# Performance work log

Hardware: AMD Instinct MI355X
Metric: run time of the kernel (lower is better)

## Reference

```python
import jax, jax.numpy as jnp
import numpy as np

B = 1024

def _back_mask(mask_out, selh, selw, s, k, hin, win):
    # Mark which input positions (of this conv) are touched by sampled k x k patches.
    hc, wc = hin - k + 1, win - k + 1
    m = np.zeros((hin, win), np.float32)
    ho, wo = mask_out.shape
    for i in range(ho):
        for j in range(wo):
            if mask_out[i, j] > 0:
                ph = min(i * s + int(selh[i, j]), hc - 1)
                pw = min(j * s + int(selw[i, j]), wc - 1)
                m[ph:ph + k, pw:pw + k] = 1.0
    return m


def setup_inputs() -> dict:
    key = jax.random.key(0)
    ks = jax.random.split(key, 10)
    rng = np.random.default_rng(1)
    # stochastic pooling offsets, top-down as in the torch forward
    selh3 = rng.integers(0, 4, (1, 1)).astype(np.int32)
    selw3 = rng.integers(0, 4, (1, 1)).astype(np.int32)
    mask3 = np.ones((1, 1), np.float32)
    mask2 = _back_mask(mask3, selh3, selw3, s=4, k=3, hin=6, win=6)
    selh2 = rng.integers(0, 2, (6, 6)).astype(np.int32)
    selw2 = rng.integers(0, 2, (6, 6)).astype(np.int32)
    mask1 = _back_mask(mask2, selh2, selw2, s=2, k=3, hin=14, win=14)
    selh1 = rng.integers(0, 2, (14, 14)).astype(np.int32)
    selw1 = rng.integers(0, 2, (14, 14)).astype(np.int32)
    sc = 0.05
    return {
        "x": jax.random.normal(ks[0], (B, 3, 32, 32), jnp.float32),
        "W1": jax.random.normal(ks[1], (200, 3, 5, 5), jnp.float32) * sc,
        "b1": jax.random.normal(ks[2], (200,), jnp.float32) * sc,
        "W2": jax.random.normal(ks[3], (400, 200, 3, 3), jnp.float32) * sc,
        "b2": jax.random.normal(ks[4], (400,), jnp.float32) * sc,
        "W3": jax.random.normal(ks[5], (800, 400, 3, 3), jnp.float32) * sc,
        "b3": jax.random.normal(ks[6], (800,), jnp.float32) * sc,
        "fc_w": jax.random.normal(ks[7], (10, 800), jnp.float32) * sc,
        "fc_b": jax.random.normal(ks[8], (10,), jnp.float32) * sc,
        "selh1": jnp.asarray(selh1), "selw1": jnp.asarray(selw1),
        "selh2": jnp.asarray(selh2), "selw2": jnp.asarray(selw2),
        "selh3": jnp.asarray(selh3), "selw3": jnp.asarray(selw3),
        "mask1": jnp.asarray(mask1), "mask2": jnp.asarray(mask2),
        "mask3": jnp.asarray(mask3),
    }


def _sconv_avg(x, W, b, selh, selw, mask, k, s):
    # Stochastic conv+avgpool: compute stride-1 conv only at one sampled location
    # per pooling window, zero at masked-out output positions.
    Bq, C, H, Wd = x.shape
    hc, wc = H - k + 1, Wd - k + 1
    ho, wo = selh.shape
    ph = jnp.minimum(jnp.arange(ho)[:, None] * s + selh, hc - 1)  # (ho,wo)
    pw = jnp.minimum(jnp.arange(wo)[None, :] * s + selw, wc - 1)
    rows = ph[:, :, :, None] if False else (ph[..., None] + jnp.arange(k))  # (ho,wo,k)
    cols = pw[..., None] + jnp.arange(k)                                    # (ho,wo,k)
    # gather sampled k x k patches -> (B,C,ho,wo,k,k)
    patch = x[:, :, rows[:, :, :, None], cols[:, :, None, :]]
    out = jnp.einsum('bcxyij,ocij->boxy', patch, W) + b[None, :, None, None]
    return out * mask[None, None, :, :]


def reference(x, W1, b1, W2, b2, W3, b3, fc_w, fc_b,
              selh1, selw1, selh2, selw2, selh3, selw3,
              mask1, mask2, mask3):
    h = jax.nn.relu(_sconv_avg(x, W1, b1, selh1, selw1, mask1, k=5, s=2))   # (B,200,14,14)
    h = jax.nn.relu(_sconv_avg(h, W2, b2, selh2, selw2, mask2, k=3, s=2))   # (B,400,6,6)
    h = jax.nn.relu(_sconv_avg(h, W3, b3, selh3, selw3, mask3, k=3, s=4))   # (B,800,1,1)
    h = h.reshape(h.shape[0], -1)                                           # (B,800)
    return h @ fc_w.T + fc_b
```

## Files before the change

kernel.cpp:

```cpp
#include <hip/hip_runtime.h>


#define H1B_OFF 0ULL
#define W2B_OFF 80281600ULL
#define P3_OFF  81944576ULL
#define W3B_OFF 89415680ULL
#define H3_OFF  95485952ULL
#define W1T_OFF 98762752ULL

typedef unsigned short u16;
typedef short bf16x8 __attribute__((ext_vector_type(8)));
typedef float f32x4 __attribute__((ext_vector_type(4)));

__device__ __forceinline__ u16 f2bf(float f) {
    union { float f; unsigned int u; } v; v.f = f;
    unsigned int u = v.u + 0x7FFFu + ((v.u >> 16) & 1u);
    return (u16)(u >> 16);
}

__global__ __launch_bounds__(256) void wprep(
    const float* __restrict__ W1, const float* __restrict__ W2, const float* __restrict__ W3,
    float* __restrict__ W1t, u16* __restrict__ W2b, u16* __restrict__ W3b)
{
    int idx = blockIdx.x * 256 + threadIdx.x;
    if (idx < 20480) {
        int kk = idx / 256, oc = idx % 256;
        float v = 0.0f;
        if (oc < 200 && kk < 75) v = W1[oc * 75 + kk];
        W1t[idx] = v;
    } else if (idx < 20480 + 831488) {
        int j = idx - 20480;
        int oc = j / 1856, kk = j % 1856;
        float v = 0.0f;
        if (oc < 400 && kk < 1800) {
            int k3 = kk / 200, c = kk % 200;
            v = W2[oc * 1800 + c * 9 + k3];
        }
        W2b[j] = f2bf(v);
    } else if (idx < 20480 + 831488 + 3035136) {
        int j = idx - 20480 - 831488;
        int oc = j / 3648, kk = j % 3648;
        float v = 0.0f;
        if (oc < 800 && kk < 3600) {
            int k3 = kk / 400, c = kk % 400;
            v = W3[oc * 3600 + c * 9 + k3];
        }
        W3b[j] = f2bf(v);
    }
}

__global__ __launch_bounds__(256) void l1_kernel(
    const float* __restrict__ x, const float* __restrict__ W1t, const float* __restrict__ b1,
    const int* __restrict__ selh, const int* __restrict__ selw, const float* __restrict__ mask,
    u16* __restrict__ h1b)
{
    const int pos = blockIdx.x;
    const float m = mask[pos];
    if (m == 0.0f) return;
    const int i = pos / 14, j = pos % 14;
    const int b0 = blockIdx.y * 16;
    const int tid = threadIdx.x;
    const int ph = min(i * 2 + selh[pos], 27);
    const int pw = min(j * 2 + selw[pos], 27);

    __shared__ __align__(16) float patch[16 * 80];
    for (int e = tid; e < 1280; e += 256) {
        int u = e / 80, kk = e % 80;
        float v = 0.0f;
        if (kk < 75) {
            int c = kk / 25, d = kk % 25;
            v = x[((size_t)(b0 + u) * 3 + c) * 1024 + (ph + d / 5) * 32 + (pw + d % 5)];
        }
        patch[e] = v;
    }
    __syncthreads();

    const int g = tid & 63;
    const int us = tid >> 6;
    const float4* w4 = reinterpret_cast<const float4*>(W1t);
    const float4* p4 = reinterpret_cast<const float4*>(patch);

    float4 acc[4];
#pragma unroll
    for (int uu = 0; uu < 4; ++uu) acc[uu] = make_float4(0.f, 0.f, 0.f, 0.f);

#pragma unroll 2
    for (int q = 0; q < 20; ++q) {
        float4 w0 = w4[(q * 4 + 0) * 64 + g];
        float4 w1 = w4[(q * 4 + 1) * 64 + g];
        float4 w2 = w4[(q * 4 + 2) * 64 + g];
        float4 w3 = w4[(q * 4 + 3) * 64 + g];
#pragma unroll
        for (int uu = 0; uu < 4; ++uu) {
            float4 p = p4[(us * 4 + uu) * 20 + q];
            acc[uu].x = fmaf(w0.x, p.x, acc[uu].x);
            acc[uu].y = fmaf(w0.y, p.x, acc[uu].y);
            acc[uu].z = fmaf(w0.z, p.x, acc[uu].z);
            acc[uu].w = fmaf(w0.w, p.x, acc[uu].w);
            acc[uu].x = fmaf(w1.x, p.y, acc[uu].x);
            acc[uu].y = fmaf(w1.y, p.y, acc[uu].y);
            acc[uu].z = fmaf(w1.z, p.y, acc[uu].z);
            acc[uu].w = fmaf(w1.w, p.y, acc[uu].w);
            acc[uu].x = fmaf(w2.x, p.z, acc[uu].x);
            acc[uu].y = fmaf(w2.y, p.z, acc[uu].y);
            acc[uu].z = fmaf(w2.z, p.z, acc[uu].z);
            acc[uu].w = fmaf(w2.w, p.z, acc[uu].w);
            acc[uu].x = fmaf(w3.x, p.w, acc[uu].x);
            acc[uu].y = fmaf(w3.y, p.w, acc[uu].y);
            acc[uu].z = fmaf(w3.z, p.w, acc[uu].z);
            acc[uu].w = fmaf(w3.w, p.w, acc[uu].w);
        }
    }

    if (g < 50) {
        float4 bv = reinterpret_cast<const float4*>(b1)[g];
#pragma unroll
        for (int uu = 0; uu < 4; ++uu) {
            int b = b0 + us * 4 + uu;
            ushort4 o;
            o.x = f2bf(fmaxf((acc[uu].x + bv.x) * m, 0.0f));
            o.y = f2bf(fmaxf((acc[uu].y + bv.y) * m, 0.0f));
            o.z = f2bf(fmaxf((acc[uu].z + bv.z) * m, 0.0f));
            o.w = f2bf(fmaxf((acc[uu].w + bv.w) * m, 0.0f));
            *reinterpret_cast<ushort4*>(&h1b[((size_t)b * 196 + pos) * 200 + g * 4]) = o;
        }
    }
}

__global__ __launch_bounds__(256) void gemm_l2(
    const u16* __restrict__ h1b, const u16* __restrict__ B, const float* __restrict__ bias,
    const int* __restrict__ selh2, const int* __restrict__ selw2,
    const int* __restrict__ selh3, const int* __restrict__ selw3,
    u16* __restrict__ P3)
{
    const int KP = 1856, NKT = 29;
    const int m0 = blockIdx.x * 64, n0 = blockIdx.y * 64;
    const int tid = threadIdx.x;
    const int lane = tid & 63, wid = tid >> 6;
    const int wm = wid >> 1, wn = wid & 1;

    __shared__ u16 Asm[64][72];
    __shared__ u16 Bsm[64][72];

    f32x4 zero = {0.f, 0.f, 0.f, 0.f};
    f32x4 acc00 = zero, acc01 = zero, acc10 = zero, acc11 = zero;

    const int ar = tid >> 3, ac = tid & 7;
    const int ph2 = min(selh3[0], 3), pw2 = min(selw3[0], 3);
    int mr0 = m0 + ar, mr1 = mr0 + 32;
    int bq0 = mr0 / 9, p0 = mr0 - bq0 * 9;
    int bq1 = mr1 / 9, p1 = mr1 - bq1 * 9;
    int pos0 = (ph2 + p0 / 3) * 6 + (pw2 + p0 % 3);
    int pos1 = (ph2 + p1 / 3) * 6 + (pw2 + p1 % 3);
    int base0 = bq0 * 196 + min(2 * (pos0 / 6) + selh2[pos0], 11) * 14
                          + min(2 * (pos0 % 6) + selw2[pos0], 11);
    int base1 = bq1 * 196 + min(2 * (pos1 / 6) + selh2[pos1], 11) * 14
                          + min(2 * (pos1 % 6) + selw2[pos1], 11);
    auto gatherA = [&](int kt, int base) -> uint4 {
        int chunk = kt * 8 + ac;
        if (chunk >= 225) return make_uint4(0u, 0u, 0u, 0u);
        int k3 = chunk / 25, c8 = chunk - k3 * 25;
        int srow = base + (k3 / 3) * 14 + (k3 - (k3 / 3) * 3);
        return *reinterpret_cast<const uint4*>(h1b + (size_t)srow * 200 + c8 * 8);
    };
    const uint4* Bg0 = reinterpret_cast<const uint4*>(B + (size_t)(n0 + ar) * KP + ac * 8);
    const uint4* Bg1 = reinterpret_cast<const uint4*>(B + (size_t)(n0 + ar + 32) * KP + ac * 8);
    uint4* As0 = reinterpret_cast<uint4*>(&Asm[ar][ac * 8]);
    uint4* As1 = reinterpret_cast<uint4*>(&Asm[ar + 32][ac * 8]);
    uint4* Bs0 = reinterpret_cast<uint4*>(&Bsm[ar][ac * 8]);
    uint4* Bs1 = reinterpret_cast<uint4*>(&Bsm[ar + 32][ac * 8]);

    uint4 ra0 = gatherA(0, base0), ra1 = gatherA(0, base1);
    uint4 rb0 = Bg0[0], rb1 = Bg1[0];
    const int r = lane & 15, ks = lane >> 4;
    for (int kt = 0; kt < NKT; ++kt) {
        __syncthreads();
        *As0 = ra0; *As1 = ra1; *Bs0 = rb0; *Bs1 = rb1;
        __syncthreads();
        if (kt + 1 < NKT) {
            ra0 = gatherA(kt + 1, base0); ra1 = gatherA(kt + 1, base1);
            rb0 = Bg0[(kt + 1) * 8];      rb1 = Bg1[(kt + 1) * 8];
        }
#pragma unroll
        for (int s = 0; s < 2; ++s) {
            bf16x8 a0 = *reinterpret_cast<const bf16x8*>(&Asm[wm * 32 + r][s * 32 + ks * 8]);
            bf16x8 a1 = *reinterpret_cast<const bf16x8*>(&Asm[wm * 32 + 16 + r][s * 32 + ks * 8]);
            bf16x8 b0 = *reinterpret_cast<const bf16x8*>(&Bsm[wn * 32 + r][s * 32 + ks * 8]);
            bf16x8 b1 = *reinterpret_cast<const bf16x8*>(&Bsm[wn * 32 + 16 + r][s * 32 + ks * 8]);
            acc00 = __builtin_amdgcn_mfma_f32_16x16x32_bf16(a0, b0, acc00, 0, 0, 0);
            acc01 = __builtin_amdgcn_mfma_f32_16x16x32_bf16(a0, b1, acc01, 0, 0, 0);
            acc10 = __builtin_amdgcn_mfma_f32_16x16x32_bf16(a1, b0, acc10, 0, 0, 0);
            acc11 = __builtin_amdgcn_mfma_f32_16x16x32_bf16(a1, b1, acc11, 0, 0, 0);
        }
    }
    const int colb = n0 + wn * 32 + (lane & 15);
    const int rowb = m0 + wm * 32 + ((lane >> 4) << 2);
#define L2STORE(ACC, MR, NR) { \
    int oc = colb + (NR) * 16; \
    if (oc < 400) { float bv = bias[oc]; \
        _Pragma("unroll") \
        for (int rr = 0; rr < 4; ++rr) { \
            int row = rowb + (MR) * 16 + rr; \
            int bq = row / 9, pq = row - (row / 9) * 9; \
            P3[(size_t)bq * 3648 + pq * 400 + oc] = f2bf(fmaxf(ACC[rr] + bv, 0.0f)); \
        } } }
    L2STORE(acc00, 0, 0) L2STORE(acc01, 0, 1) L2STORE(acc10, 1, 0) L2STORE(acc11, 1, 1)
#undef L2STORE
}

__global__ __launch_bounds__(256) void gemm_l3(
    const u16* __restrict__ A, const u16* __restrict__ B,
    const float* __restrict__ bias, float* __restrict__ h3)
{
    const int KP = 3648, NKT = 57;
    const int m0 = blockIdx.x * 64, n0 = blockIdx.y * 64;
    const int tid = threadIdx.x;
    const int lane = tid & 63, wid = tid >> 6;
    const int wm = wid >> 1, wn = wid & 1;

    __shared__ u16 Asm[64][72];
    __shared__ u16 Bsm[64][72];

    f32x4 zero = {0.f, 0.f, 0.f, 0.f};
    f32x4 acc00 = zero, acc01 = zero, acc10 = zero, acc11 = zero;

    const int ar = tid >> 3, ac = tid & 7;
    auto gatherA = [&](int kt, int row) -> uint4 {
        int chunk = kt * 8 + ac;
        if (chunk >= 450) return make_uint4(0u, 0u, 0u, 0u);
        return *reinterpret_cast<const uint4*>(A + (size_t)row * KP + chunk * 8);
    };
    const uint4* Bg0 = reinterpret_cast<const uint4*>(B + (size_t)(n0 + ar) * KP + ac * 8);
    const uint4* Bg1 = reinterpret_cast<const uint4*>(B + (size_t)(n0 + ar + 32) * KP + ac * 8);
    uint4* As0 = reinterpret_cast<uint4*>(&Asm[ar][ac * 8]);
    uint4* As1 = reinterpret_cast<uint4*>(&Asm[ar + 32][ac * 8]);
    uint4* Bs0 = reinterpret_cast<uint4*>(&Bsm[ar][ac * 8]);
    uint4* Bs1 = reinterpret_cast<uint4*>(&Bsm[ar + 32][ac * 8]);

    uint4 ra0 = gatherA(0, m0 + ar), ra1 = gatherA(0, m0 + ar + 32);
    uint4 rb0 = Bg0[0], rb1 = Bg1[0];
    const int r = lane & 15, ks = lane >> 4;
    for (int kt = 0; kt < NKT; ++kt) {
        __syncthreads();
        *As0 = ra0; *As1 = ra1; *Bs0 = rb0; *Bs1 = rb1;
        __syncthreads();
        if (kt + 1 < NKT) {
            ra0 = gatherA(kt + 1, m0 + ar); ra1 = gatherA(kt + 1, m0 + ar + 32);
            rb0 = Bg0[(kt + 1) * 8];        rb1 = Bg1[(kt + 1) * 8];
        }
#pragma unroll
        for (int s = 0; s < 2; ++s) {
            bf16x8 a0 = *reinterpret_cast<const bf16x8*>(&Asm[wm * 32 + r][s * 32 + ks * 8]);
            bf16x8 a1 = *reinterpret_cast<const bf16x8*>(&Asm[wm * 32 + 16 + r][s * 32 + ks * 8]);
            bf16x8 b0 = *reinterpret_cast<const bf16x8*>(&Bsm[wn * 32 + r][s * 32 + ks * 8]);
            bf16x8 b1 = *reinterpret_cast<const bf16x8*>(&Bsm[wn * 32 + 16 + r][s * 32 + ks * 8]);
            acc00 = __builtin_amdgcn_mfma_f32_16x16x32_bf16(a0, b0, acc00, 0, 0, 0);
            acc01 = __builtin_amdgcn_mfma_f32_16x16x32_bf16(a0, b1, acc01, 0, 0, 0);
            acc10 = __builtin_amdgcn_mfma_f32_16x16x32_bf16(a1, b0, acc10, 0, 0, 0);
            acc11 = __builtin_amdgcn_mfma_f32_16x16x32_bf16(a1, b1, acc11, 0, 0, 0);
        }
    }
    const int colb = n0 + wn * 32 + (lane & 15);
    const int rowb = m0 + wm * 32 + ((lane >> 4) << 2);
#define L3STORE(ACC, MR, NR) { \
    int oc = colb + (NR) * 16; \
    if (oc < 800) { float bv = bias[oc]; \
        _Pragma("unroll") \
        for (int rr = 0; rr < 4; ++rr) { \
            int row = rowb + (MR) * 16 + rr; \
            h3[(size_t)row * 800 + oc] = fmaxf(ACC[rr] + bv, 0.0f); \
        } } }
    L3STORE(acc00, 0, 0) L3STORE(acc01, 0, 1) L3STORE(acc10, 1, 0) L3STORE(acc11, 1, 1)
#undef L3STORE
}

__global__ __launch_bounds__(256) void fc_kernel(
    const float* __restrict__ h3, const float* __restrict__ fcw, const float* __restrict__ fcb,
    float* __restrict__ out)
{
    const int idx = blockIdx.x * 256 + threadIdx.x;
    if (idx >= 1024 * 10) return;
    const int b = idx / 10, o = idx % 10;
    float acc = fcb[o];
    const float4* hp = reinterpret_cast<const float4*>(h3 + b * 800);
    const float4* wp = reinterpret_cast<const float4*>(fcw + o * 800);
    for (int k = 0; k < 200; ++k) {
        float4 h = hp[k], w = wp[k];
        acc = fmaf(h.x, w.x, acc);
        acc = fmaf(h.y, w.y, acc);
        acc = fmaf(h.z, w.z, acc);
        acc = fmaf(h.w, w.w, acc);
    }
    out[idx] = acc;
}

extern "C" void kernel_launch(void* const* d_in, const int* in_sizes, int n_in,
                              void* d_out, int out_size, void* d_ws, size_t ws_size,
                              hipStream_t stream) {
    const float* x     = (const float*)d_in[0];
    const float* W1    = (const float*)d_in[1];
    const float* b1    = (const float*)d_in[2];
    const float* W2    = (const float*)d_in[3];
    const float* b2    = (const float*)d_in[4];
    const float* W3    = (const float*)d_in[5];
    const float* b3    = (const float*)d_in[6];
    const float* fc_w  = (const float*)d_in[7];
    const float* fc_b  = (const float*)d_in[8];
    const int*   selh1 = (const int*)d_in[9];
    const int*   selw1 = (const int*)d_in[10];
    const int*   selh2 = (const int*)d_in[11];
    const int*   selw2 = (const int*)d_in[12];
    const int*   selh3 = (const int*)d_in[13];
    const int*   selw3 = (const int*)d_in[14];
    const float* mask1 = (const float*)d_in[15];

    char* wsb = (char*)d_ws;
    u16*   h1b = (u16*)(wsb + H1B_OFF);
    u16*   W2b = (u16*)(wsb + W2B_OFF);
    u16*   P3  = (u16*)(wsb + P3_OFF);
    u16*   W3b = (u16*)(wsb + W3B_OFF);
    float* h3  = (float*)(wsb + H3_OFF);
    float* W1t = (float*)(wsb + W1T_OFF);
    float* out = (float*)d_out;

    wprep<<<15184, 256, 0, stream>>>(W1, W2, W3, W1t, W2b, W3b);
    l1_kernel<<<dim3(196, 64), 256, 0, stream>>>(x, W1t, b1, selh1, selw1, mask1, h1b);
    gemm_l2<<<dim3(144, 7), 256, 0, stream>>>(h1b, W2b, b2, selh2, selw2, selh3, selw3, P3);
    gemm_l3<<<dim3(16, 13), 256, 0, stream>>>(P3, W3b, b3, h3);
    fc_kernel<<<40, 256, 0, stream>>>(h3, fc_w, fc_b, out);
}
```

Baseline: 259.5 us.

## Split-K layer-3 GEMM into two halves and double l1 batch tile

gemm_l3 now runs with a z-dimension of 2, each half covering part of the K range and writing partial sums to separate buffers. The bias is added only in the first half, and the ReLU moves into fc_kernel, which sums the two partials on load. This doubles the block count of the small 208-block GEMM to fill more compute units. The price is extra global traffic for the second partial buffer. Separately, l1_kernel now handles 32 batch rows per block instead of 16, with 8 accumulators per thread, so weights are reused more at the cost of higher register pressure.

Result: faster. 243.9 us (-6.0%).

```diff
diff --git a/kernel.cpp b/kernel.cpp
--- a/kernel.cpp
+++ b/kernel.cpp
@@ -5,8 +5,9 @@
 #define W2B_OFF 80281600ULL
 #define P3_OFF  81944576ULL
 #define W3B_OFF 89415680ULL
-#define H3_OFF  95485952ULL
-#define W1T_OFF 98762752ULL
+#define H3A_OFF 95485952ULL
+#define H3B_OFF 98762752ULL
+#define W1T_OFF 102039552ULL
 
 typedef unsigned short u16;
 typedef short bf16x8 __attribute__((ext_vector_type(8)));
@@ -58,13 +59,13 @@
     const float m = mask[pos];
     if (m == 0.0f) return;
     const int i = pos / 14, j = pos % 14;
-    const int b0 = blockIdx.y * 16;
+    const int b0 = blockIdx.y * 32;
     const int tid = threadIdx.x;
     const int ph = min(i * 2 + selh[pos], 27);
     const int pw = min(j * 2 + selw[pos], 27);
 
-    __shared__ __align__(16) float patch[16 * 80];
-    for (int e = tid; e < 1280; e += 256) {
+    __shared__ __align__(16) float patch[32 * 80];
+    for (int e = tid; e < 2560; e += 256) {
         int u = e / 80, kk = e % 80;
         float v = 0.0f;
         if (kk < 75) {
@@ -80,19 +81,18 @@
     const float4* w4 = reinterpret_cast<const float4*>(W1t);
     const float4* p4 = reinterpret_cast<const float4*>(patch);
 
-    float4 acc[4];
-#pragma unroll
-    for (int uu = 0; uu < 4; ++uu) acc[uu] = make_float4(0.f, 0.f, 0.f, 0.f);
-
-#pragma unroll 2
+    float4 acc[8];
+#pragma unroll
+    for (int uu = 0; uu < 8; ++uu) acc[uu] = make_float4(0.f, 0.f, 0.f, 0.f);
+
     for (int q = 0; q < 20; ++q) {
         float4 w0 = w4[(q * 4 + 0) * 64 + g];
         float4 w1 = w4[(q * 4 + 1) * 64 + g];
         float4 w2 = w4[(q * 4 + 2) * 64 + g];
         float4 w3 = w4[(q * 4 + 3) * 64 + g];
 #pragma unroll
-        for (int uu = 0; uu < 4; ++uu) {
-            float4 p = p4[(us * 4 + uu) * 20 + q];
+        for (int uu = 0; uu < 8; ++uu) {
+            float4 p = p4[(us * 8 + uu) * 20 + q];
             acc[uu].x = fmaf(w0.x, p.x, acc[uu].x);
             acc[uu].y = fmaf(w0.y, p.x, acc[uu].y);
             acc[uu].z = fmaf(w0.z, p.x, acc[uu].z);
@@ -115,8 +115,8 @@
     if (g < 50) {
         float4 bv = reinterpret_cast<const float4*>(b1)[g];
 #pragma unroll
-        for (int uu = 0; uu < 4; ++uu) {
-            int b = b0 + us * 4 + uu;
+        for (int uu = 0; uu < 8; ++uu) {
+            int b = b0 + us * 8 + uu;
             ushort4 o;
             o.x = f2bf(fmaxf((acc[uu].x + bv.x) * m, 0.0f));
             o.y = f2bf(fmaxf((acc[uu].y + bv.y) * m, 0.0f));
@@ -210,9 +210,12 @@
 
 __global__ __launch_bounds__(256) void gemm_l3(
     const u16* __restrict__ A, const u16* __restrict__ B,
-    const float* __restrict__ bias, float* __restrict__ h3)
-{
-    const int KP = 3648, NKT = 57;
+    const float* __restrict__ bias, float* __restrict__ h3a, float* __restrict__ h3b)
+{
+    const int KP = 3648;
+    const int z = blockIdx.z;
+    const int kt0 = z ? 28 : 0;
+    const int NKT = z ? 29 : 28;
     const int m0 = blockIdx.x * 64, n0 = blockIdx.y * 64;
     const int tid = threadIdx.x;
     const int lane = tid & 63, wid = tid >> 6;
@@ -237,16 +240,16 @@
     uint4* Bs0 = reinterpret_cast<uint4*>(&Bsm[ar][ac * 8]);
     uint4* Bs1 = reinterpret_cast<uint4*>(&Bsm[ar + 32][ac * 8]);
 
-    uint4 ra0 = gatherA(0, m0 + ar), ra1 = gatherA(0, m0 + ar + 32);
-    uint4 rb0 = Bg0[0], rb1 = Bg1[0];
+    uint4 ra0 = gatherA(kt0, m0 + ar), ra1 = gatherA(kt0, m0 + ar + 32);
+    uint4 rb0 = Bg0[kt0 * 8], rb1 = Bg1[kt0 * 8];
     const int r = lane & 15, ks = lane >> 4;
     for (int kt = 0; kt < NKT; ++kt) {
         __syncthreads();
         *As0 = ra0; *As1 = ra1; *Bs0 = rb0; *Bs1 = rb1;
         __syncthreads();
         if (kt + 1 < NKT) {
-            ra0 = gatherA(kt + 1, m0 + ar); ra1 = gatherA(kt + 1, m0 + ar + 32);
-            rb0 = Bg0[(kt + 1) * 8];        rb1 = Bg1[(kt + 1) * 8];
+            ra0 = gatherA(kt0 + kt + 1, m0 + ar); ra1 = gatherA(kt0 + kt + 1, m0 + ar + 32);
+            rb0 = Bg0[(kt0 + kt + 1) * 8];        rb1 = Bg1[(kt0 + kt + 1) * 8];
         }
 #pragma unroll
         for (int s = 0; s < 2; ++s) {
@@ -262,34 +265,37 @@
     }
     const int colb = n0 + wn * 32 + (lane & 15);
     const int rowb = m0 + wm * 32 + ((lane >> 4) << 2);
+    float* dst = z ? h3b : h3a;
 #define L3STORE(ACC, MR, NR) { \
     int oc = colb + (NR) * 16; \
-    if (oc < 800) { float bv = bias[oc]; \
+    if (oc < 800) { float bv = z ? 0.0f : bias[oc]; \
         _Pragma("unroll") \
         for (int rr = 0; rr < 4; ++rr) { \
             int row = rowb + (MR) * 16 + rr; \
-            h3[(size_t)row * 800 + oc] = fmaxf(ACC[rr] + bv, 0.0f); \
+            dst[(size_t)row * 800 + oc] = ACC[rr] + bv; \
         } } }
     L3STORE(acc00, 0, 0) L3STORE(acc01, 0, 1) L3STORE(acc10, 1, 0) L3STORE(acc11, 1, 1)
 #undef L3STORE
 }
 
 __global__ __launch_bounds__(256) void fc_kernel(
-    const float* __restrict__ h3, const float* __restrict__ fcw, const float* __restrict__ fcb,
+    const float* __restrict__ h3a, const float* __restrict__ h3b,
+    const float* __restrict__ fcw, const float* __restrict__ fcb,
     float* __restrict__ out)
 {
     const int idx = blockIdx.x * 256 + threadIdx.x;
     if (idx >= 1024 * 10) return;
     const int b = idx / 10, o = idx % 10;
     float acc = fcb[o];
-    const float4* hp = reinterpret_cast<const float4*>(h3 + b * 800);
-    const float4* wp = reinterpret_cast<const float4*>(fcw + o * 800);
+    const float4* hp0 = reinterpret_cast<const float4*>(h3a + b * 800);
+    const float4* hp1 = reinterpret_cast<const float4*>(h3b + b * 800);
+    const float4* wp  = reinterpret_cast<const float4*>(fcw + o * 800);
     for (int k = 0; k < 200; ++k) {
-        float4 h = hp[k], w = wp[k];
-        acc = fmaf(h.x, w.x, acc);
-        acc = fmaf(h.y, w.y, acc);
-        acc = fmaf(h.z, w.z, acc);
-        acc = fmaf(h.w, w.w, acc);
+        float4 p0 = hp0[k], p1 = hp1[k], w = wp[k];
+        acc = fmaf(fmaxf(p0.x + p1.x, 0.0f), w.x, acc);
+        acc = fmaf(fmaxf(p0.y + p1.y, 0.0f), w.y, acc);
+        acc = fmaf(fmaxf(p0.z + p1.z, 0.0f), w.z, acc);
+        acc = fmaf(fmaxf(p0.w + p1.w, 0.0f), w.w, acc);
     }
     out[idx] = acc;
 }
@@ -319,13 +325,14 @@
     u16*   W2b = (u16*)(wsb + W2B_OFF);
     u16*   P3  = (u16*)(wsb + P3_OFF);
     u16*   W3b = (u16*)(wsb + W3B_OFF);
-    float* h3  = (float*)(wsb + H3_OFF);
+    float* h3a = (float*)(wsb + H3A_OFF);
+    float* h3b = (float*)(wsb + H3B_OFF);
     float* W1t = (float*)(wsb + W1T_OFF);
     float* out = (float*)d_out;
 
     wprep<<<15184, 256, 0, stream>>>(W1, W2, W3, W1t, W2b, W3b);
-    l1_kernel<<<dim3(196, 64), 256, 0, stream>>>(x, W1t, b1, selh1, selw1, mask1, h1b);
+    l1_kernel<<<dim3(196, 32), 256, 0, stream>>>(x, W1t, b1, selh1, selw1, mask1, h1b);
     gemm_l2<<<dim3(144, 7), 256, 0, stream>>>(h1b, W2b, b2, selh2, selw2, selh3, selw3, P3);
-    gemm_l3<<<dim3(16, 13), 256, 0, stream>>>(P3, W3b, b3, h3);
-    fc_kernel<<<40, 256, 0, stream>>>(h3, fc_w, fc_b, out);
-}
+    gemm_l3<<<dim3(16, 13, 2), 256, 0, stream>>>(P3, W3b, b3, h3a, h3b);
+    fc_kernel<<<40, 256, 0, stream>>>(h3a, h3b, fc_w, fc_b, out);
+}
```
